# Kernel optimization log

Hardware: AMD Instinct MI355X
Metric: run time of the kernel (lower is better)

Reference implementation:

```python
import jax, jax.numpy as jnp
import numpy as np

B, S, D = 128, 1024, 64
H, O = 128, 512
NUM_FEATURES = 7  # 5 + 2 (wobble)
COUPLING = -1.0          # set explicitly in __init__: self.c.coupling = -1.0
WOBBLE_STEP = 0.015625   # wb += 0.015625 each step (from forward)
WOBBLE_AMP = 0.25        # wobble drive amplitude inside accumulator (assumed)
WOBBLE_COUPLING = 0.25   # wb relaxation rate on repeated inputs (assumed)


def setup_inputs() -> dict:
    key = jax.random.key(0)
    k0, k1, k2, k3 = jax.random.split(key, 4)
    def lin(k, out_d, in_d):
        return jax.random.normal(k, (out_d, in_d), jnp.float32) / np.sqrt(in_d).astype(np.float32)
    return {
        "x": jax.random.normal(k0, (B, S, D), jnp.float32),
        "We": lin(k1, H, D),                      # encoder Linear(input_dim, hidden)
        "be": jnp.zeros((H,), jnp.float32),
        "omega": 0.1 * jax.random.normal(k2, (H,), jnp.float32),  # natural frequency
        "Wr": lin(k3, O, NUM_FEATURES * H),       # readout Linear(7*hidden, output_dim)
        "br": jnp.zeros((O,), jnp.float32),
    }


def reference(x, We, be, omega, Wr, br):
    Bn, Sn, Dn = x.shape
    Hn = We.shape[0]
    ph0 = jnp.zeros((Bn, Hn), x.dtype)
    wb0 = jnp.zeros((Bn, Hn), x.dtype)
    prev0 = jnp.full((Bn, Dn), jnp.inf, x.dtype)  # inf != any finite xt -> first step is_repeat=False

    def step(carry, xt):
        ph, wb, prev = carry
        pt = xt @ We.T + be                                   # [B,H] encoded phase
        # xpt = stack([cos(pt), sin(pt)]) -> target angle (wrapped to (-pi,pi])
        theta = jnp.arctan2(jnp.sin(pt), jnp.cos(pt))
        wb = wb + WOBBLE_STEP
        is_rep = jnp.all(xt == prev)                          # scalar bool (replaces .item())
        # phase accumulator update (Kuramoto-style with wobble drive)
        ph_new = ph + omega + COUPLING * jnp.sin(theta - ph) + WOBBLE_AMP * jnp.sin(wb)
        # wobble state only updated by accumulator on repeated inputs
        wb_new = jnp.where(is_rep, wb + WOBBLE_COUPLING * jnp.sin(theta - wb), wb)
        ph_s = 0.5 * ph_new
        feats = jnp.concatenate([
            jnp.cos(ph_new), jnp.sin(ph_new),
            jnp.cos(ph_s), jnp.sin(ph_s),
            jnp.cos(wb_new), jnp.sin(wb_new),
            ph_new,
        ], axis=1)                                            # [B, 7H]
        logits = feats @ Wr.T + br                            # [B, O]
        return (ph_new, wb_new, xt), (logits, ph_new, wb_new)

    _, (logits, ph_hist, wb_hist) = jax.lax.scan(step, (ph0, wb0, prev0), jnp.swapaxes(x, 0, 1))
    # [S,B,...] -> [B,S,...]
    return (jnp.swapaxes(logits, 0, 1), jnp.swapaxes(ph_hist, 0, 1), jnp.swapaxes(wb_hist, 0, 1))
```

## Files before the change

### kernel.cpp

```cpp
#include <hip/hip_runtime.h>
#include <math.h>

#define S_LEN 1024
#define B_DIM 128
#define D_DIM 64
#define H_DIM 128
#define O_DIM 512
#define M_DIM 131072

__global__ __launch_bounds__(256) void enc_kernel(
    const float* __restrict__ x, const float* __restrict__ We,
    const float* __restrict__ be, float* __restrict__ pt) {
  __shared__ __align__(16) float xs[1024];
  int tid = threadIdx.x;
  long q0 = (long)blockIdx.x * 16;
  for (int i = tid; i < 1024; i += 256) xs[i] = x[q0 * 64 + i];
  __syncthreads();
  int h = tid & 127;
  int pg = tid >> 7;
  float4 w[16];
  const float4* w4 = (const float4*)(We + (long)h * 64);
#pragma unroll
  for (int i = 0; i < 16; ++i) w[i] = w4[i];
  float bias = be[h];
#pragma unroll
  for (int j = 0; j < 8; ++j) {
    int p = pg * 8 + j;
    const float4* x4 = (const float4*)(xs + p * 64);
    float acc = 0.f;
#pragma unroll
    for (int i = 0; i < 16; ++i) {
      float4 a = x4[i];
      float4 b = w[i];
      acc += a.x * b.x + a.y * b.y + a.z * b.z + a.w * b.w;
    }
    long q = q0 + p;
    int bb = (int)(q >> 10), t = (int)(q & 1023);
    pt[(long)t * 16384 + bb * 128 + h] = acc + bias;
  }
}

__global__ __launch_bounds__(256) void rep_kernel(const float* __restrict__ x,
                                                  int* __restrict__ rep) {
  int t = blockIdx.x;
  int tid = threadIdx.x;
  if (t == 0) {
    if (tid == 0) rep[0] = 0;
    return;
  }
  int ok = 1;
  for (int j = tid; j < B_DIM * D_DIM; j += 256) {
    int b = j >> 6, d = j & 63;
    long i1 = (long)b * S_LEN * 64 + (long)t * 64 + d;
    if (x[i1] != x[i1 - 64]) ok = 0;
  }
  ok = __syncthreads_and(ok);
  if (tid == 0) rep[t] = ok;
}

__global__ __launch_bounds__(64) void scan_kernel(
    const float* __restrict__ pt, const float* __restrict__ omega,
    const int* __restrict__ rep, float* __restrict__ ph_out,
    float* __restrict__ wb_out) {
  __shared__ int reps[1024];
  int tid = threadIdx.x;
  for (int i = tid; i < 1024; i += 64) reps[i] = rep[i];
  __syncthreads();
  int g = blockIdx.x * 64 + tid;
  int b = g >> 7, h = g & 127;
  float om = omega[h];
  float ph = 0.f, wb = 0.f;
  long obase = (long)b * (S_LEN * 128) + h;
  float cur[16], nxt[16];
#pragma unroll
  for (int u = 0; u < 16; ++u) cur[u] = pt[(long)u * 16384 + g];
  for (int t0 = 0; t0 < S_LEN; t0 += 16) {
#pragma unroll
    for (int u = 0; u < 16; ++u) {
      int tl = t0 + 16 + u;
      if (tl > 1023) tl = 1023;
      nxt[u] = pt[(long)tl * 16384 + g];
    }
#pragma unroll
    for (int u = 0; u < 16; ++u) {
      int t = t0 + u;
      float th = cur[u];
      wb += 0.015625f;
      ph = ph + om - sinf(th - ph) + 0.25f * sinf(wb);
      if (reps[t]) wb = wb + 0.25f * sinf(th - wb);
      ph_out[obase + (long)t * 128] = ph;
      wb_out[obase + (long)t * 128] = wb;
    }
#pragma unroll
    for (int u = 0; u < 16; ++u) cur[u] = nxt[u];
  }
}

typedef short bf16x8 __attribute__((ext_vector_type(8)));
typedef float f32x4 __attribute__((ext_vector_type(4)));

__device__ __forceinline__ unsigned short bf_rne(float x) {
  union { float f; unsigned u; } c;
  c.f = x;
  unsigned u = c.u;
  return (unsigned short)((u + 0x7fffu + ((u >> 16) & 1u)) >> 16);
}
__device__ __forceinline__ float bf_to_f(unsigned short h) {
  union { unsigned u; float f; } c;
  c.u = ((unsigned)h) << 16;
  return c.f;
}

__device__ unsigned short g_Wrb[64 * 8192];

__global__ __launch_bounds__(256) void prep_wrb(const float* __restrict__ Wr) {
  int tile = blockIdx.x;
  int cb = tile >> 4;
  int c = tile & 15;
  int half = (c >> 3) & 1;
  int j = c & 7;
  const int fmap[8] = {6, 6, 2, 3, 0, 1, 4, 5};
  int f = fmap[j];
  int tid = threadIdx.x;
  int row = tid >> 1;
  int k0 = (tid & 1) * 32;
  const float* src = Wr + (long)(cb * 128 + row) * 896 + f * 128 + half * 64 + k0;
  unsigned short* dst = g_Wrb + (long)tile * 8192 + row * 64 + k0;
  int lo = (j == 1);
#pragma unroll
  for (int i = 0; i < 8; ++i) {
    float4 v = *(const float4*)&src[i * 4];
    float e[4] = {v.x, v.y, v.z, v.w};
    unsigned short q[4];
#pragma unroll
    for (int t = 0; t < 4; ++t) {
      unsigned short hb = bf_rne(e[t]);
      q[t] = lo ? bf_rne(e[t] - bf_to_f(hb)) : hb;
    }
    uint2 p;
    p.x = (unsigned)q[0] | ((unsigned)q[1] << 16);
    p.y = (unsigned)q[2] | ((unsigned)q[3] << 16);
    *(uint2*)&dst[i * 4] = p;
  }
}

__global__ __launch_bounds__(256, 2) void out_mfma(
    const float* __restrict__ ph_hist, const float* __restrict__ wb_hist,
    const float* __restrict__ br, float* __restrict__ out) {
  __shared__ __align__(16) unsigned short As0[128 * 72];
  __shared__ __align__(16) unsigned short As1[128 * 72];
  __shared__ __align__(16) unsigned short Bs0[128 * 72];
  __shared__ __align__(16) unsigned short Bs1[128 * 72];
  int tid = threadIdx.x;
  int lane = tid & 63;
  int wid = tid >> 6;
  int wm = wid >> 1, wn = wid & 1;
  int nb = ((blockIdx.x & 7) << 9) | (blockIdx.x >> 3);
  long rBlock = (long)(nb >> 2) * 128;
  int cb = nb & 3;
  int oBlock = cb * 128;
  int l15 = lane & 15;
  int kq = lane >> 4;
  int jq = tid & 15;
  int r0 = tid >> 4;
  int brow = tid >> 1;
  int bk = (tid & 1) * 32;

  const unsigned short* wsrc = g_Wrb + (long)cb * (16 * 8192);

  f32x4 acc[4][4];
#pragma unroll
  for (int mi = 0; mi < 4; ++mi)
#pragma unroll
    for (int ni = 0; ni < 4; ++ni) {
      acc[mi][ni][0] = 0.f; acc[mi][ni][1] = 0.f;
      acc[mi][ni][2] = 0.f; acc[mi][ni][3] = 0.f;
    }

  uint4 breg[8];
  auto loadB = [&](int p) {
    const uint4* s0 = (const uint4*)(wsrc + (long)(2 * p) * 8192 + tid * 32);
    const uint4* s1 = (const uint4*)(wsrc + (long)(2 * p + 1) * 8192 + tid * 32);
#pragma unroll
    for (int i = 0; i < 4; ++i) breg[i] = s0[i];
#pragma unroll
    for (int i = 0; i < 4; ++i) breg[4 + i] = s1[i];
  };
  auto writeB = [&]() {
#pragma unroll
    for (int i = 0; i < 4; ++i)
      *(uint4*)&Bs0[brow * 72 + bk + i * 8] = breg[i];
#pragma unroll
    for (int i = 0; i < 4; ++i)
      *(uint4*)&Bs1[brow * 72 + bk + i * 8] = breg[4 + i];
  };
  auto storeA = [&](int i, uint2 v0, uint2 v1) {
    *(uint2*)&As0[(r0 + 16 * i) * 72 + 4 * jq] = v0;
    *(uint2*)&As1[(r0 + 16 * i) * 72 + 4 * jq] = v1;
  };
  auto pk = [&](float a, float b) -> unsigned {
    return (unsigned)bf_rne(a) | ((unsigned)bf_rne(b) << 16);
  };
  auto mm = [&](const unsigned short* A, const unsigned short* Bsl) {
    __builtin_amdgcn_s_setprio(1);
#pragma unroll
    for (int ks = 0; ks < 2; ++ks) {
      int kk = ks * 32 + kq * 8;
      bf16x8 a[4], b[4];
#pragma unroll
      for (int mi = 0; mi < 4; ++mi)
        a[mi] = *(const bf16x8*)&A[(wm * 64 + mi * 16 + l15) * 72 + kk];
#pragma unroll
      for (int ni = 0; ni < 4; ++ni)
        b[ni] = *(const bf16x8*)&Bsl[(wn * 64 + ni * 16 + l15) * 72 + kk];
#pragma unroll
      for (int mi = 0; mi < 4; ++mi)
#pragma unroll
        for (int ni = 0; ni < 4; ++ni)
          acc[mi][ni] = __builtin_amdgcn_mfma_f32_16x16x32_bf16(
              a[mi], b[ni], acc[mi][ni], 0, 0, 0);
    }
    __builtin_amdgcn_s_setprio(0);
  };

  float4 pha[8];
#pragma unroll
  for (int i = 0; i < 8; ++i)
    pha[i] = *(const float4*)&ph_hist[(rBlock + r0 + 16 * i) * 128 + 4 * jq];
  loadB(0);

#pragma unroll
  for (int half = 0; half < 2; ++half) {
    int h0 = half * 64;
    int pb = half * 4;

    __syncthreads();
    writeB();
#pragma unroll
    for (int i = 0; i < 8; ++i) {
      float e[4] = {pha[i].x, pha[i].y, pha[i].z, pha[i].w};
      unsigned short hb[4], lb[4];
#pragma unroll
      for (int t = 0; t < 4; ++t) {
        hb[t] = bf_rne(e[t]);
        lb[t] = bf_rne(e[t] - bf_to_f(hb[t]));
      }
      uint2 vh, vl;
      vh.x = (unsigned)hb[0] | ((unsigned)hb[1] << 16);
      vh.y = (unsigned)hb[2] | ((unsigned)hb[3] << 16);
      vl.x = (unsigned)lb[0] | ((unsigned)lb[1] << 16);
      vl.y = (unsigned)lb[2] | ((unsigned)lb[3] << 16);
      storeA(i, vh, vl);
    }
    loadB(pb + 1);
    __syncthreads();
    mm(As0, Bs0);
    mm(As1, Bs0);
    mm(As0, Bs1);

    __syncthreads();
    writeB();
    uint2 f0p[8], f1p[8];
#pragma unroll
    for (int i = 0; i < 8; ++i) {
      float e[4] = {pha[i].x, pha[i].y, pha[i].z, pha[i].w};
      float s2[4], c2[4], cf[4], sf[4];
#pragma unroll
      for (int t = 0; t < 4; ++t) {
        __sincosf(0.5f * e[t], &s2[t], &c2[t]);
        cf[t] = fmaf(-2.f * s2[t], s2[t], 1.f);
        sf[t] = 2.f * s2[t] * c2[t];
      }
      uint2 vc, vs;
      vc.x = pk(c2[0], c2[1]); vc.y = pk(c2[2], c2[3]);
      vs.x = pk(s2[0], s2[1]); vs.y = pk(s2[2], s2[3]);
      storeA(i, vc, vs);
      f0p[i].x = pk(cf[0], cf[1]); f0p[i].y = pk(cf[2], cf[3]);
      f1p[i].x = pk(sf[0], sf[1]); f1p[i].y = pk(sf[2], sf[3]);
    }
    loadB(pb + 2);
    __syncthreads();
    mm(As0, Bs0);
    mm(As1, Bs1);

    __syncthreads();
    writeB();
#pragma unroll
    for (int i = 0; i < 8; ++i) storeA(i, f0p[i], f1p[i]);
#pragma unroll
    for (int i = 0; i < 8; ++i)
      pha[i] = *(const float4*)&wb_hist[(rBlock + r0 + 16 * i) * 128 + h0 + 4 * jq];
    loadB(pb + 3);
    __syncthreads();
    mm(As0, Bs0);
    mm(As1, Bs1);

    __syncthreads();
    writeB();
#pragma unroll
    for (int i = 0; i < 8; ++i) {
      float e[4] = {pha[i].x, pha[i].y, pha[i].z, pha[i].w};
      float sn[4], cs[4];
#pragma unroll
      for (int t = 0; t < 4; ++t) __sincosf(e[t], &sn[t], &cs[t]);
      uint2 vc, vs;
      vc.x = pk(cs[0], cs[1]); vc.y = pk(cs[2], cs[3]);
      vs.x = pk(sn[0], sn[1]); vs.y = pk(sn[2], sn[3]);
      storeA(i, vc, vs);
    }
    if (half == 0) {
#pragma unroll
      for (int i = 0; i < 8; ++i)
        pha[i] = *(const float4*)&ph_hist[(rBlock + r0 + 16 * i) * 128 + 64 + 4 * jq];
      loadB(4);
    }
    __syncthreads();
    mm(As0, Bs0);
    mm(As1, Bs1);
  }

  __syncthreads();
  float* ep = (float*)(wn == 0 ? (void*)Bs0 : (void*)Bs1) + wm * 1152;
  float4 br4 = *(const float4*)&br[oBlock + wn * 64 + l15 * 4];
#pragma unroll
  for (int mi = 0; mi < 4; ++mi) {
#pragma unroll
    for (int ni = 0; ni < 4; ++ni)
#pragma unroll
      for (int r = 0; r < 4; ++r)
        ep[(kq * 4 + r) * 68 + ni * 16 + l15] = acc[mi][ni][r];
#pragma unroll
    for (int p = 0; p < 4; ++p) {
      int row = p * 4 + kq;
      float4 v = *(const float4*)&ep[row * 68 + l15 * 4];
      v.x += br4.x; v.y += br4.y; v.z += br4.z; v.w += br4.w;
      long grow = rBlock + wm * 64 + mi * 16 + row;
      *(float4*)&out[grow * 512 + oBlock + wn * 64 + l15 * 4] = v;
    }
  }
}

extern "C" void kernel_launch(void* const* d_in, const int* in_sizes, int n_in,
                              void* d_out, int out_size, void* d_ws,
                              size_t ws_size, hipStream_t stream) {
  (void)in_sizes; (void)n_in; (void)d_ws; (void)ws_size; (void)out_size;
  const float* x = (const float*)d_in[0];
  const float* We = (const float*)d_in[1];
  const float* be = (const float*)d_in[2];
  const float* omega = (const float*)d_in[3];
  const float* Wr = (const float*)d_in[4];
  const float* br = (const float*)d_in[5];

  float* out = (float*)d_out;
  float* logits = out;
  float* ph_hist = out + (long)M_DIM * O_DIM;
  float* wb_hist = ph_hist + (long)M_DIM * H_DIM;

  float* pt = logits;
  int* rep = (int*)(logits + 40l * 1024 * 1024);

  prep_wrb<<<64, 256, 0, stream>>>(Wr);
  enc_kernel<<<M_DIM / 16, 256, 0, stream>>>(x, We, be, pt);
  rep_kernel<<<S_LEN, 256, 0, stream>>>(x, rep);
  scan_kernel<<<256, 64, 0, stream>>>(pt, omega, rep, ph_hist, wb_hist);
  out_mfma<<<4096, 256, 0, stream>>>(ph_hist, wb_hist, br, logits);
}
```

Before: 1.128 ms.

## Stage readout weights directly into LDS with XOR-swizzled layout

Replaces the register-staged global-to-LDS copy of the bf16 readout weight tiles with direct global_load_lds transfers, and precomputes an XOR swizzle on the weight layout during prep so the unpadded 64-wide LDS rows avoid bank conflicts on MFMA operand reads. This removes the VGPR cost of the breg buffer and the separate LDS write instructions. In exchange, the prefetch that previously overlapped each weight load with the preceding MFMA phase is gone, so loads are now issued right after the barrier and waited on before compute, which may expose latency. Correctness relies on the vmcnt wait being placed before the barrier.

```diff
diff --git a/kernel.cpp b/kernel.cpp
--- a/kernel.cpp
+++ b/kernel.cpp
@@ -124,8 +124,9 @@
   int tid = threadIdx.x;
   int row = tid >> 1;
   int k0 = (tid & 1) * 32;
+  int xr = (row & 7) << 3;
   const float* src = Wr + (long)(cb * 128 + row) * 896 + f * 128 + half * 64 + k0;
-  unsigned short* dst = g_Wrb + (long)tile * 8192 + row * 64 + k0;
+  unsigned short* dst = g_Wrb + (long)tile * 8192 + row * 64;
   int lo = (j == 1);
 #pragma unroll
   for (int i = 0; i < 8; ++i) {
@@ -140,17 +141,20 @@
     uint2 p;
     p.x = (unsigned)q[0] | ((unsigned)q[1] << 16);
     p.y = (unsigned)q[2] | ((unsigned)q[3] << 16);
-    *(uint2*)&dst[i * 4] = p;
-  }
-}
+    *(uint2*)&dst[(k0 + i * 4) ^ xr] = p;
+  }
+}
+
+typedef const void __attribute__((address_space(1))) gas_void;
+typedef void __attribute__((address_space(3))) las_void;
 
 __global__ __launch_bounds__(256, 2) void out_mfma(
     const float* __restrict__ ph_hist, const float* __restrict__ wb_hist,
     const float* __restrict__ br, float* __restrict__ out) {
   __shared__ __align__(16) unsigned short As0[128 * 72];
   __shared__ __align__(16) unsigned short As1[128 * 72];
-  __shared__ __align__(16) unsigned short Bs0[128 * 72];
-  __shared__ __align__(16) unsigned short Bs1[128 * 72];
+  __shared__ __align__(16) unsigned short Bs0[128 * 64];
+  __shared__ __align__(16) unsigned short Bs1[128 * 64];
   int tid = threadIdx.x;
   int lane = tid & 63;
   int wid = tid >> 6;
@@ -163,8 +167,6 @@
   int kq = lane >> 4;
   int jq = tid & 15;
   int r0 = tid >> 4;
-  int brow = tid >> 1;
-  int bk = (tid & 1) * 32;
 
   const unsigned short* wsrc = g_Wrb + (long)cb * (16 * 8192);
 
@@ -177,22 +179,18 @@
       acc[mi][ni][2] = 0.f; acc[mi][ni][3] = 0.f;
     }
 
-  uint4 breg[8];
-  auto loadB = [&](int p) {
-    const uint4* s0 = (const uint4*)(wsrc + (long)(2 * p) * 8192 + tid * 32);
-    const uint4* s1 = (const uint4*)(wsrc + (long)(2 * p + 1) * 8192 + tid * 32);
-#pragma unroll
-    for (int i = 0; i < 4; ++i) breg[i] = s0[i];
-#pragma unroll
-    for (int i = 0; i < 4; ++i) breg[4 + i] = s1[i];
-  };
-  auto writeB = [&]() {
-#pragma unroll
-    for (int i = 0; i < 4; ++i)
-      *(uint4*)&Bs0[brow * 72 + bk + i * 8] = breg[i];
-#pragma unroll
-    for (int i = 0; i < 4; ++i)
-      *(uint4*)&Bs1[brow * 72 + bk + i * 8] = breg[4 + i];
+  auto stageB = [&](int p) {
+    const unsigned short* t0 = wsrc + (long)(2 * p) * 8192;
+    const unsigned short* t1 = wsrc + (long)(2 * p + 1) * 8192;
+#pragma unroll
+    for (int q = 0; q < 4; ++q) {
+      int c = wid * 4 + q;
+      int so = c * 512 + lane * 8;
+      __builtin_amdgcn_global_load_lds((gas_void*)(t0 + so),
+                                       (las_void*)(Bs0 + c * 512), 16, 0, 0);
+      __builtin_amdgcn_global_load_lds((gas_void*)(t1 + so),
+                                       (las_void*)(Bs1 + c * 512), 16, 0, 0);
+    }
   };
   auto storeA = [&](int i, uint2 v0, uint2 v1) {
     *(uint2*)&As0[(r0 + 16 * i) * 72 + 4 * jq] = v0;
@@ -201,6 +199,7 @@
   auto pk = [&](float a, float b) -> unsigned {
     return (unsigned)bf_rne(a) | ((unsigned)bf_rne(b) << 16);
   };
+  int xr = (l15 & 7) << 3;
   auto mm = [&](const unsigned short* A, const unsigned short* Bsl) {
     __builtin_amdgcn_s_setprio(1);
 #pragma unroll
@@ -212,7 +211,7 @@
         a[mi] = *(const bf16x8*)&A[(wm * 64 + mi * 16 + l15) * 72 + kk];
 #pragma unroll
       for (int ni = 0; ni < 4; ++ni)
-        b[ni] = *(const bf16x8*)&Bsl[(wn * 64 + ni * 16 + l15) * 72 + kk];
+        b[ni] = *(const bf16x8*)&Bsl[(wn * 64 + ni * 16 + l15) * 64 + (kk ^ xr)];
 #pragma unroll
       for (int mi = 0; mi < 4; ++mi)
 #pragma unroll
@@ -227,7 +226,6 @@
 #pragma unroll
   for (int i = 0; i < 8; ++i)
     pha[i] = *(const float4*)&ph_hist[(rBlock + r0 + 16 * i) * 128 + 4 * jq];
-  loadB(0);
 
 #pragma unroll
   for (int half = 0; half < 2; ++half) {
@@ -235,7 +233,7 @@
     int pb = half * 4;
 
     __syncthreads();
-    writeB();
+    stageB(pb + 0);
 #pragma unroll
     for (int i = 0; i < 8; ++i) {
       float e[4] = {pha[i].x, pha[i].y, pha[i].z, pha[i].w};
@@ -252,14 +250,13 @@
       vl.y = (unsigned)lb[2] | ((unsigned)lb[3] << 16);
       storeA(i, vh, vl);
     }
-    loadB(pb + 1);
     __syncthreads();
     mm(As0, Bs0);
     mm(As1, Bs0);
     mm(As0, Bs1);
 
     __syncthreads();
-    writeB();
+    stageB(pb + 1);
     uint2 f0p[8], f1p[8];
 #pragma unroll
     for (int i = 0; i < 8; ++i) {
@@ -278,25 +275,23 @@
       f0p[i].x = pk(cf[0], cf[1]); f0p[i].y = pk(cf[2], cf[3]);
       f1p[i].x = pk(sf[0], sf[1]); f1p[i].y = pk(sf[2], sf[3]);
     }
-    loadB(pb + 2);
     __syncthreads();
     mm(As0, Bs0);
     mm(As1, Bs1);
 
     __syncthreads();
-    writeB();
+    stageB(pb + 2);
 #pragma unroll
     for (int i = 0; i < 8; ++i) storeA(i, f0p[i], f1p[i]);
 #pragma unroll
     for (int i = 0; i < 8; ++i)
       pha[i] = *(const float4*)&wb_hist[(rBlock + r0 + 16 * i) * 128 + h0 + 4 * jq];
-    loadB(pb + 3);
     __syncthreads();
     mm(As0, Bs0);
     mm(As1, Bs1);
 
     __syncthreads();
-    writeB();
+    stageB(pb + 3);
 #pragma unroll
     for (int i = 0; i < 8; ++i) {
       float e[4] = {pha[i].x, pha[i].y, pha[i].z, pha[i].w};
@@ -312,7 +307,6 @@
 #pragma unroll
       for (int i = 0; i < 8; ++i)
         pha[i] = *(const float4*)&ph_hist[(rBlock + r0 + 16 * i) * 128 + 64 + 4 * jq];
-      loadB(4);
     }
     __syncthreads();
     mm(As0, Bs0);
```

After: 903.6 us. 1.25x faster.
